# Optimization experiments

Hardware: AMD Instinct MI355X
Metric: run time of the kernel (lower is better)

The kernel has to match this reference:

```python
import jax, jax.numpy as jnp
import numpy as np

TAU = 2.0
V_TH = 1.0
PI = float(np.pi)
T = 3

@jax.custom_vjp
def spike(x):
    # Heaviside spike; backward uses ATan surrogate (alpha=2.0) as in spikingjelly
    return (x >= 0.0).astype(x.dtype)

def _spike_fwd(x):
    return spike(x), x

def _spike_bwd(x, g):
    # d/dx of (1/pi) atan(pi/2 * alpha * x) + 1/2 with alpha=2 => 1/(1+(pi*x)^2)
    return (g / (1.0 + (PI * x) ** 2),)

spike.defvjp(_spike_fwd, _spike_bwd)

def lif_step(v, x):
    # decay_input=True, v_reset=0.0 hard reset: v += (x - v)/tau
    v = v + (x - v) / TAU
    s = spike(v - V_TH)
    v = v * (1.0 - s)
    return v, s

def setup_inputs() -> dict:
    key = jax.random.key(0)
    ks = jax.random.split(key, 7)
    B, D, H, O = 16384, 2752, 256, 100
    dvs = jax.random.normal(ks[0], (B, T, D), dtype=jnp.float32)
    W1 = jax.random.normal(ks[1], (H, D), dtype=jnp.float32) * (1.0 / np.sqrt(D))
    b1 = jnp.zeros((H,), dtype=jnp.float32)
    W2 = jax.random.normal(ks[2], (H, H), dtype=jnp.float32) * (1.0 / np.sqrt(H))
    b2 = jnp.zeros((H,), dtype=jnp.float32)
    W3 = jax.random.normal(ks[3], (O, H), dtype=jnp.float32) * (1.0 / np.sqrt(H))
    b3 = jnp.zeros((O,), dtype=jnp.float32)
    return {"dvs": dvs, "W1": W1, "b1": b1, "W2": W2, "b2": b2, "W3": W3, "b3": b3}

def reference(dvs, W1, b1, W2, b2, W3, b3):
    # dvs: [B, T, D] -> [T, B, D]
    x_tbd = jnp.swapaxes(dvs, 0, 1)
    B = dvs.shape[0]
    v1 = jnp.zeros((B, W1.shape[0]), dtype=dvs.dtype)
    v2 = jnp.zeros((B, W2.shape[0]), dtype=dvs.dtype)
    v3 = jnp.zeros((B, W3.shape[0]), dtype=dvs.dtype)
    out = None
    for t in range(T):  # fixed T=3, state carried across steps
        h = x_tbd[t] @ W1.T + b1
        v1, s1 = lif_step(v1, h)
        h = s1 @ W2.T + b2
        v2, s2 = lif_step(v2, h)
        h = s2 @ W3.T + b3
        v3, s3 = lif_step(v3, h)
        out = s3
    return out  # spikes at last timestep, [B, 100]
```

## Files before the change

### kernel.cpp

```cpp
#include <hip/hip_runtime.h>

#define B_SZ    16384
#define T_STEPS 3
#define D_IN    2752
#define H_SZ    256
#define O_SZ    100
#define LDA     (T_STEPS * D_IN)

typedef short bf16x8 __attribute__((ext_vector_type(8)));
typedef float f32x4  __attribute__((ext_vector_type(4)));

__device__ __forceinline__ unsigned short f2bf(float x) {
  union { float f; unsigned int u; } v; v.f = x;
  unsigned int r = v.u + 0x7FFFu + ((v.u >> 16) & 1u);
  return (unsigned short)(r >> 16);
}

__global__ void cvt_w1_kernel(const float* __restrict__ W1,
                              unsigned short* __restrict__ W1bf) {
  int i = (blockIdx.x * 256 + threadIdx.x) * 4;
  float4 v = *(const float4*)(W1 + i);
  unsigned short o[4] = {f2bf(v.x), f2bf(v.y), f2bf(v.z), f2bf(v.w)};
  *(uint2*)(W1bf + i) = *(uint2*)o;
}

#define BM 64
#define BN 256
#define BK 32
#define LDK 40

__global__ __launch_bounds__(256) void gemm1_mfma_kernel(
    const float* __restrict__ dvs, const unsigned short* __restrict__ W1bf,
    const float* __restrict__ b1, float* __restrict__ Hout) {
  __shared__ unsigned short At[BM][LDK];
  __shared__ unsigned short Bt[BN][LDK];

  const int r0   = blockIdx.x * BM;
  const int t    = r0 >> 14;
  const int brow = r0 & (B_SZ - 1);
  const float* Abase = dvs + (size_t)brow * LDA + t * D_IN;

  const int tid  = threadIdx.x;
  const int lane = tid & 63, wv = tid >> 6;
  const int wn0  = wv * 64;
  const int lrow = lane & 15;
  const int kgrp = lane >> 4;

  const int s_row = tid >> 2;
  const int s_kq  = (tid & 3) << 3;
  const float* ap0 = Abase + (size_t)s_row * LDA + s_kq;
  const unsigned short* bp0 = W1bf + (size_t)tid * D_IN;

  f32x4 acc[4][4] = {};

  for (int k0 = 0; k0 < D_IN; k0 += BK) {
    float4 a0 = *(const float4*)(ap0 + k0);
    float4 a1 = *(const float4*)(ap0 + k0 + 4);
    uint4 bv0 = *(const uint4*)(bp0 + k0);
    uint4 bv1 = *(const uint4*)(bp0 + k0 + 8);
    uint4 bv2 = *(const uint4*)(bp0 + k0 + 16);
    uint4 bv3 = *(const uint4*)(bp0 + k0 + 24);

    __syncthreads();

    unsigned short a8[8] = {f2bf(a0.x), f2bf(a0.y), f2bf(a0.z), f2bf(a0.w),
                            f2bf(a1.x), f2bf(a1.y), f2bf(a1.z), f2bf(a1.w)};
    *(uint4*)&At[s_row][s_kq] = *(uint4*)a8;
    *(uint4*)&Bt[tid][0]  = bv0;
    *(uint4*)&Bt[tid][8]  = bv1;
    *(uint4*)&Bt[tid][16] = bv2;
    *(uint4*)&Bt[tid][24] = bv3;

    __syncthreads();

    bf16x8 af[4], bfr[4];
#pragma unroll
    for (int m = 0; m < 4; m++)
      af[m] = *(const bf16x8*)&At[m * 16 + lrow][kgrp * 8];
#pragma unroll
    for (int n = 0; n < 4; n++)
      bfr[n] = *(const bf16x8*)&Bt[wn0 + n * 16 + lrow][kgrp * 8];
#pragma unroll
    for (int m = 0; m < 4; m++)
#pragma unroll
      for (int n = 0; n < 4; n++)
        acc[m][n] = __builtin_amdgcn_mfma_f32_16x16x32_bf16(
            af[m], bfr[n], acc[m][n], 0, 0, 0);
  }

#pragma unroll
  for (int m = 0; m < 4; m++) {
    int gm = r0 + m * 16 + kgrp * 4;
#pragma unroll
    for (int n = 0; n < 4; n++) {
      int gn = wn0 + n * 16 + lrow;
      float bias = b1[gn];
#pragma unroll
      for (int r = 0; r < 4; r++)
        Hout[(size_t)(gm + r) * H_SZ + gn] = acc[m][n][r] + bias;
    }
  }
}

__global__ void transpose_kernel(const float* __restrict__ in,
                                 float* __restrict__ out, int rows, int cols) {
  __shared__ float tile[32][33];
  int bc = blockIdx.x * 32, br = blockIdx.y * 32;
  int tx = threadIdx.x, ty = threadIdx.y;
  for (int j = 0; j < 32; j += 8) {
    int r = br + ty + j, c = bc + tx;
    if (r < rows && c < cols) tile[ty + j][tx] = in[(size_t)r * cols + c];
  }
  __syncthreads();
  for (int j = 0; j < 32; j += 8) {
    int c = bc + ty + j, r = br + tx;
    if (c < cols && r < rows) out[(size_t)c * rows + r] = tile[tx][ty + j];
  }
}

__global__ __launch_bounds__(256) void recurrent2_kernel(
    const float* __restrict__ H, const float* __restrict__ W2T,
    const float* __restrict__ b2, const float* __restrict__ W3T,
    const float* __restrict__ b3, float* __restrict__ out) {
  const int tid = threadIdx.x, lane = tid & 63, wv = tid >> 6;
  const int b0 = blockIdx.x * 32 + wv * 8;

  float b2v[4];
#pragma unroll
  for (int q = 0; q < 4; q++) b2v[q] = b2[lane + 64 * q];
  const float b3a = b3[lane];
  const float b3b = (lane < O_SZ - 64) ? b3[64 + lane] : 0.f;

  for (int bi = 0; bi < 8; bi++) {
    const int b = b0 + bi;
    float v1[4] = {0.f, 0.f, 0.f, 0.f};
    float v2[4] = {0.f, 0.f, 0.f, 0.f};
    float v3a = 0.f, v3b = 0.f, s3a = 0.f, s3b = 0.f;

    for (int t = 0; t < T_STEPS; t++) {
      const float* hp = H + ((size_t)t * B_SZ + b) * H_SZ;
      unsigned long long m1[4];
      float h2[4] = {b2v[0], b2v[1], b2v[2], b2v[3]};
#pragma unroll
      for (int q = 0; q < 4; q++) {
        float h1 = hp[lane + 64 * q];
        v1[q] = 0.5f * (v1[q] + h1);
        bool s = (v1[q] >= 1.0f);
        m1[q] = __ballot(s);
        if (s) v1[q] = 0.f;
      }
#pragma unroll
      for (int q = 0; q < 4; q++) {
        unsigned long long m = m1[q];
        while (m) {
          int n = 64 * q + __builtin_ctzll(m);
          m &= m - 1;
          const float* wp = W2T + (size_t)n * H_SZ + lane;
          h2[0] += wp[0]; h2[1] += wp[64]; h2[2] += wp[128]; h2[3] += wp[192];
        }
      }
      unsigned long long m2[4];
#pragma unroll
      for (int q = 0; q < 4; q++) {
        v2[q] = 0.5f * (v2[q] + h2[q]);
        bool s = (v2[q] >= 1.0f);
        m2[q] = __ballot(s);
        if (s) v2[q] = 0.f;
      }
      float h3a = b3a, h3b = b3b;
#pragma unroll
      for (int q = 0; q < 4; q++) {
        unsigned long long m = m2[q];
        while (m) {
          int j = 64 * q + __builtin_ctzll(m);
          m &= m - 1;
          h3a += W3T[(size_t)j * O_SZ + lane];
          if (lane < O_SZ - 64) h3b += W3T[(size_t)j * O_SZ + 64 + lane];
        }
      }
      v3a = 0.5f * (v3a + h3a);
      v3b = 0.5f * (v3b + h3b);
      bool sa = (v3a >= 1.0f), sb = (v3b >= 1.0f);
      if (sa) v3a = 0.f;
      if (sb) v3b = 0.f;
      if (t == T_STEPS - 1) { s3a = sa ? 1.f : 0.f; s3b = sb ? 1.f : 0.f; }
    }
    out[(size_t)b * O_SZ + lane] = s3a;
    if (lane < O_SZ - 64) out[(size_t)b * O_SZ + 64 + lane] = s3b;
  }
}

extern "C" void kernel_launch(void* const* d_in, const int* in_sizes, int n_in,
                              void* d_out, int out_size, void* d_ws, size_t ws_size,
                              hipStream_t stream) {
  const float* dvs = (const float*)d_in[0];
  const float* W1  = (const float*)d_in[1];
  const float* b1  = (const float*)d_in[2];
  const float* W2  = (const float*)d_in[3];
  const float* b2  = (const float*)d_in[4];
  const float* W3  = (const float*)d_in[5];
  const float* b3  = (const float*)d_in[6];
  float* out = (float*)d_out;

  char* ws = (char*)d_ws;
  float* Hbuf = (float*)ws;
  float* W2T  = (float*)(ws + (size_t)T_STEPS * B_SZ * H_SZ * 4);
  float* W3T  = W2T + H_SZ * H_SZ;
  unsigned short* W1bf = (unsigned short*)(W3T + H_SZ * O_SZ);

  dim3 tb(32, 8);
  hipLaunchKernelGGL(cvt_w1_kernel, dim3((H_SZ * D_IN) / 1024), dim3(256),
                     0, stream, W1, W1bf);
  hipLaunchKernelGGL(transpose_kernel, dim3(8, 8), tb, 0, stream, W2, W2T, H_SZ, H_SZ);
  hipLaunchKernelGGL(transpose_kernel, dim3(8, 4), tb, 0, stream, W3, W3T, O_SZ, H_SZ);
  hipLaunchKernelGGL(gemm1_mfma_kernel, dim3((T_STEPS * B_SZ) / BM), dim3(256),
                     0, stream, dvs, W1bf, b1, Hbuf);
  hipLaunchKernelGGL(recurrent2_kernel, dim3(B_SZ / 32), dim3(256), 0, stream,
                     Hbuf, W2T, b2, W3T, b3, out);
}
```

Before: 944.5 us.

## Double-buffer GEMM1 with direct global-to-LDS B loads and more recurrent blocks

GEMM1 now double-buffers its A and B tiles in LDS. The B (bf16 W1) tiles are loaded with global_load_lds straight into a swizzled LDS layout, and the next tile is prefetched while MFMAs run on the current one, so global latency is hidden and there is one barrier per iteration. Launch bounds ask for 3 blocks per SM. Separately, the recurrent kernel now handles 8 batch rows per block instead of 32, giving four times as many blocks and better occupancy. The price is more LDS per block and swizzle logic that has to match exactly.

Result: faster. 835.5 us (-11.5%).

```diff
diff --git a/kernel.cpp b/kernel.cpp
--- a/kernel.cpp
+++ b/kernel.cpp
@@ -16,6 +16,12 @@
   return (unsigned short)(r >> 16);
 }
 
+__device__ __forceinline__ void gload_lds16(const void* g, void* l) {
+  __builtin_amdgcn_global_load_lds(
+      (const __attribute__((address_space(1))) unsigned int*)g,
+      (__attribute__((address_space(3))) unsigned int*)l, 16, 0, 0);
+}
+
 __global__ void cvt_w1_kernel(const float* __restrict__ W1,
                               unsigned short* __restrict__ W1bf) {
   int i = (blockIdx.x * 256 + threadIdx.x) * 4;
@@ -27,13 +33,28 @@
 #define BM 64
 #define BN 256
 #define BK 32
+#define NT (D_IN / BK)
 #define LDK 40
 
-__global__ __launch_bounds__(256) void gemm1_mfma_kernel(
+__device__ __forceinline__ void stage_B(const unsigned short* __restrict__ W1bf,
+                                        unsigned short (*Bbuf)[BK],
+                                        int k0, int tid) {
+  const int lane = tid & 63, w = tid >> 6;
+#pragma unroll
+  for (int q = 0; q < 4; ++q) {
+    int g = (w * 4 + q) * 64 + lane;
+    int r = g >> 2, c = g & 3;
+    int cp = c ^ ((r >> 1) & 3);
+    const unsigned short* src = W1bf + (size_t)r * D_IN + k0 + cp * 8;
+    gload_lds16(src, &Bbuf[(w * 4 + q) * 16][0]);
+  }
+}
+
+__global__ __launch_bounds__(256, 3) void gemm1_mfma_kernel(
     const float* __restrict__ dvs, const unsigned short* __restrict__ W1bf,
     const float* __restrict__ b1, float* __restrict__ Hout) {
-  __shared__ unsigned short At[BM][LDK];
-  __shared__ unsigned short Bt[BN][LDK];
+  __shared__ __attribute__((aligned(16))) unsigned short Ab[2][BM][LDK];
+  __shared__ __attribute__((aligned(16))) unsigned short Bb[2][BN][BK];
 
   const int r0   = blockIdx.x * BM;
   const int t    = r0 >> 14;
@@ -45,47 +66,60 @@
   const int wn0  = wv * 64;
   const int lrow = lane & 15;
   const int kgrp = lane >> 4;
+  const int pidx = kgrp ^ ((lrow >> 1) & 3);
 
   const int s_row = tid >> 2;
   const int s_kq  = (tid & 3) << 3;
   const float* ap0 = Abase + (size_t)s_row * LDA + s_kq;
-  const unsigned short* bp0 = W1bf + (size_t)tid * D_IN;
 
   f32x4 acc[4][4] = {};
 
-  for (int k0 = 0; k0 < D_IN; k0 += BK) {
-    float4 a0 = *(const float4*)(ap0 + k0);
-    float4 a1 = *(const float4*)(ap0 + k0 + 4);
-    uint4 bv0 = *(const uint4*)(bp0 + k0);
-    uint4 bv1 = *(const uint4*)(bp0 + k0 + 8);
-    uint4 bv2 = *(const uint4*)(bp0 + k0 + 16);
-    uint4 bv3 = *(const uint4*)(bp0 + k0 + 24);
-
-    __syncthreads();
-
+  {
+    float4 a0 = *(const float4*)(ap0);
+    float4 a1 = *(const float4*)(ap0 + 4);
+    stage_B(W1bf, Bb[0], 0, tid);
     unsigned short a8[8] = {f2bf(a0.x), f2bf(a0.y), f2bf(a0.z), f2bf(a0.w),
                             f2bf(a1.x), f2bf(a1.y), f2bf(a1.z), f2bf(a1.w)};
-    *(uint4*)&At[s_row][s_kq] = *(uint4*)a8;
-    *(uint4*)&Bt[tid][0]  = bv0;
-    *(uint4*)&Bt[tid][8]  = bv1;
-    *(uint4*)&Bt[tid][16] = bv2;
-    *(uint4*)&Bt[tid][24] = bv3;
-
+    *(uint4*)&Ab[0][s_row][s_kq] = *(uint4*)a8;
+  }
+  __syncthreads();
+
+  int cur = 0;
+  for (int k = 0; k < NT; ++k) {
+    const bool pf = (k + 1 < NT);
+    float4 a0n, a1n;
+    if (pf) {
+      const int k0n = (k + 1) * BK;
+      a0n = *(const float4*)(ap0 + k0n);
+      a1n = *(const float4*)(ap0 + k0n + 4);
+      stage_B(W1bf, Bb[cur ^ 1], k0n, tid);
+    }
+
+    {
+      const unsigned short (*Ac)[LDK] = Ab[cur];
+      const unsigned short (*Bc)[BK]  = Bb[cur];
+      bf16x8 af[4], bfr[4];
+#pragma unroll
+      for (int m = 0; m < 4; m++)
+        af[m] = *(const bf16x8*)&Ac[m * 16 + lrow][kgrp * 8];
+#pragma unroll
+      for (int n = 0; n < 4; n++)
+        bfr[n] = *(const bf16x8*)&Bc[wn0 + n * 16 + lrow][pidx * 8];
+#pragma unroll
+      for (int m = 0; m < 4; m++)
+#pragma unroll
+        for (int n = 0; n < 4; n++)
+          acc[m][n] = __builtin_amdgcn_mfma_f32_16x16x32_bf16(
+              af[m], bfr[n], acc[m][n], 0, 0, 0);
+    }
+
+    if (pf) {
+      unsigned short a8[8] = {f2bf(a0n.x), f2bf(a0n.y), f2bf(a0n.z), f2bf(a0n.w),
+                              f2bf(a1n.x), f2bf(a1n.y), f2bf(a1n.z), f2bf(a1n.w)};
+      *(uint4*)&Ab[cur ^ 1][s_row][s_kq] = *(uint4*)a8;
+    }
     __syncthreads();
-
-    bf16x8 af[4], bfr[4];
-#pragma unroll
-    for (int m = 0; m < 4; m++)
-      af[m] = *(const bf16x8*)&At[m * 16 + lrow][kgrp * 8];
-#pragma unroll
-    for (int n = 0; n < 4; n++)
-      bfr[n] = *(const bf16x8*)&Bt[wn0 + n * 16 + lrow][kgrp * 8];
-#pragma unroll
-    for (int m = 0; m < 4; m++)
-#pragma unroll
-      for (int n = 0; n < 4; n++)
-        acc[m][n] = __builtin_amdgcn_mfma_f32_16x16x32_bf16(
-            af[m], bfr[n], acc[m][n], 0, 0, 0);
+    cur ^= 1;
   }
 
 #pragma unroll
@@ -123,7 +157,7 @@
     const float* __restrict__ b2, const float* __restrict__ W3T,
     const float* __restrict__ b3, float* __restrict__ out) {
   const int tid = threadIdx.x, lane = tid & 63, wv = tid >> 6;
-  const int b0 = blockIdx.x * 32 + wv * 8;
+  const int b0 = blockIdx.x * 8 + wv * 2;
 
   float b2v[4];
 #pragma unroll
@@ -131,7 +165,7 @@
   const float b3a = b3[lane];
   const float b3b = (lane < O_SZ - 64) ? b3[64 + lane] : 0.f;
 
-  for (int bi = 0; bi < 8; bi++) {
+  for (int bi = 0; bi < 2; bi++) {
     const int b = b0 + bi;
     float v1[4] = {0.f, 0.f, 0.f, 0.f};
     float v2[4] = {0.f, 0.f, 0.f, 0.f};
@@ -215,6 +249,6 @@
   hipLaunchKernelGGL(transpose_kernel, dim3(8, 4), tb, 0, stream, W3, W3T, O_SZ, H_SZ);
   hipLaunchKernelGGL(gemm1_mfma_kernel, dim3((T_STEPS * B_SZ) / BM), dim3(256),
                      0, stream, dvs, W1bf, b1, Hbuf);
-  hipLaunchKernelGGL(recurrent2_kernel, dim3(B_SZ / 32), dim3(256), 0, stream,
+  hipLaunchKernelGGL(recurrent2_kernel, dim3(B_SZ / 8), dim3(256), 0, stream,
                      Hbuf, W2T, b2, W3T, b3, out);
 }
```
